# Kernel optimization log

Measured on AMD Instinct MI355X. Metric: run time of the kernel, lower is better.

Reference implementation:

```python
import jax, jax.numpy as jnp
import numpy as np

N, C, T, V, D = 64, 64, 256, 25, 64
BN_EPS = 1e-5


def _make_shift(v, ch, sign):
    idx = np.empty(v * ch, dtype=np.int64)
    for i in range(v):
        for j in range(ch):
            idx[i * ch + j] = (i * ch + j + sign * j * ch) % (ch * v)
    return jnp.asarray(idx, dtype=jnp.int32)


def setup_inputs() -> dict:
    key = jax.random.key(0)
    ks = jax.random.split(key, 8)
    return {
        "x0": jax.random.normal(ks[0], (N, C, T, V), dtype=jnp.float32),
        "fc1_w": jax.random.normal(ks[1], (C // 4, C), dtype=jnp.float32) * (1.0 / np.sqrt(C)),
        "fc1_b": jnp.zeros((C // 4,), dtype=jnp.float32),
        "fc2_w": jax.random.normal(ks[2], (4, C // 4), dtype=jnp.float32) * (1.0 / np.sqrt(C // 4)),
        "fc2_b": jnp.zeros((4,), dtype=jnp.float32),
        "Linear_weight": jax.random.normal(ks[3], (4, C, D), dtype=jnp.float32) * np.sqrt(1.0 / D),
        "Linear_bias": jax.random.normal(ks[4], (4, D), dtype=jnp.float32) * 0.02,
        "Feature_Mask": jax.random.normal(ks[5], (1, V, C), dtype=jnp.float32) * 0.1,
        "bn_gamma": 1.0 + 0.05 * jax.random.normal(ks[6], (V * D,), dtype=jnp.float32),
        "bn_beta": 0.05 * jax.random.normal(ks[7], (V * D,), dtype=jnp.float32),
        "shift_in": _make_shift(V, C, +1),
        "shift_out": _make_shift(V, D, -1),
        "epoch": 100,
    }


def reference(x0, fc1_w, fc1_b, fc2_w, fc2_b, Linear_weight, Linear_bias,
              Feature_Mask, bn_gamma, bn_beta, shift_in, shift_out, epoch):
    n, c, t, v = x0.shape
    d = Linear_weight.shape[-1]

    # DY_SEModule gate: global avg pool -> 1x1 convs -> tempered softmax over 4
    pooled = x0.mean(axis=(2, 3))                       # [n, c]
    h = jax.nn.relu(pooled @ fc1_w.T + fc1_b)           # [n, c//4]
    logits = h @ fc2_w.T + fc2_b                        # [n, 4]
    tao = (-(30.0 - 1.0) / 60.0 * epoch + 30.0) if epoch < 60 else 1.0
    gate = jax.nn.softmax(logits / tao, axis=1)         # [n, 4]

    # per-sample fused weights / bias
    W_fuse = jnp.einsum('kcd,nk->ncd', Linear_weight, gate)   # [n, c, d]
    b_fuse = jnp.einsum('kc,nk->nc', Linear_bias, gate)       # [n, d]

    # shift-in gather over flattened (v*c) channel axis
    x = x0.transpose(0, 2, 3, 1).reshape(n * t, v * c)  # [n*t, v*c]
    x = x[:, shift_in].reshape(n * t, v, c)
    x = x * (jnp.tanh(Feature_Mask) + 1.0)              # learnable feature mask
    x = x.reshape(n, t, v, c)

    # per-sample dynamic linear + bias
    x = jnp.einsum('ntvc,ncd->ntvd', x, W_fuse) + b_fuse[:, None, None, :]

    # shift-out gather
    x = x.reshape(n * t, v * d)[:, shift_out]           # [n*t, v*d]

    # BatchNorm1d (training mode: batch statistics over n*t)
    mean = x.mean(axis=0)
    var = jnp.var(x, axis=0)
    x = (x - mean) * jax.lax.rsqrt(var + BN_EPS) * bn_gamma + bn_beta

    x = x.reshape(n, t, v, d).transpose(0, 3, 1, 2)     # [n, d, t, v]
    return jax.nn.relu(x + x0)                          # identity residual (c == d)
```

## Files before the change

### kernel.cpp

```cpp
#include <hip/hip_runtime.h>
#include <hip/hip_bf16.h>
#include <math.h>

#define NN 64
#define CC 64
#define TT 256
#define VV 25
#define DD 64
#define BN_EPS 1e-5f

typedef short bf16x8 __attribute__((ext_vector_type(8)));
typedef float f32x4 __attribute__((ext_vector_type(4)));

#define WS_POOLED 0
#define WS_GATE   4096
#define WS_BFUSE  4352
#define WS_MASK   8448
#define WS_ABP    10048
#define WS_PART2  13248
#define WS_WTB    218048
#define WS_YB     349120

static __device__ __forceinline__ unsigned short f2bf(float x) {
    __hip_bfloat16 h = __float2bfloat16(x);
    return *(unsigned short*)&h;
}
static __device__ __forceinline__ float bf2f(unsigned short u) {
    return __uint_as_float(((unsigned)u) << 16);
}

__global__ __launch_bounds__(256) void k_mask(const float* __restrict__ fmask, float* ws) {
    const int f = blockIdx.x * 256 + threadIdx.x;
    if (f < VV * CC) ws[WS_MASK + f] = tanhf(fmask[f]) + 1.0f;
}

__global__ __launch_bounds__(256) void k_pool(const float* __restrict__ x0,
                                              float* __restrict__ pooled) {
    __shared__ float red[256];
    const int bid = blockIdx.x;
    const float4* p = (const float4*)(x0 + (size_t)bid * (TT * VV));
    float s = 0.f;
    for (int k = threadIdx.x; k < (TT * VV) / 4; k += 256) {
        float4 v = p[k];
        s += v.x + v.y + v.z + v.w;
    }
    red[threadIdx.x] = s;
    __syncthreads();
    for (int off = 128; off > 0; off >>= 1) {
        if (threadIdx.x < off) red[threadIdx.x] += red[threadIdx.x + off];
        __syncthreads();
    }
    if (threadIdx.x == 0) pooled[bid] = red[0] * (1.f / (TT * VV));
}

__global__ __launch_bounds__(256) void k_gate(const float* __restrict__ fc1_w,
                                              const float* __restrict__ fc1_b,
                                              const float* __restrict__ fc2_w,
                                              const float* __restrict__ fc2_b,
                                              const float* __restrict__ lin_b,
                                              const int* __restrict__ epoch_p,
                                              float* ws) {
    const int tid = threadIdx.x;
    float* pooled = ws + WS_POOLED;
    float* gate   = ws + WS_GATE;
    float* bfuse  = ws + WS_BFUSE;

    if (tid < 64) {
        const int n = tid;
        const float* po = pooled + n * 64;
        float h[16];
        for (int q = 0; q < 16; q++) {
            float z = fc1_b[q];
            for (int j = 0; j < 64; j++) z = fmaf(fc1_w[q * 64 + j], po[j], z);
            h[q] = fmaxf(z, 0.f);
        }
        float lg[4];
        for (int k = 0; k < 4; k++) {
            float z = fc2_b[k];
            for (int q = 0; q < 16; q++) z = fmaf(fc2_w[k * 16 + q], h[q], z);
            lg[k] = z;
        }
        const int ep = epoch_p[0];
        const float tao = (ep < 60) ? (-(29.0f / 60.0f) * (float)ep + 30.0f) : 1.0f;
        float mx = -1e30f;
        for (int k = 0; k < 4; k++) { lg[k] /= tao; mx = fmaxf(mx, lg[k]); }
        float se = 0.f;
        for (int k = 0; k < 4; k++) { lg[k] = expf(lg[k] - mx); se += lg[k]; }
        const float inv = 1.f / se;
        for (int k = 0; k < 4; k++) gate[n * 4 + k] = lg[k] * inv;
    }
    __syncthreads();
    for (int f = tid; f < 4096; f += 256) {
        const int n = f >> 6, d = f & 63;
        float s = 0.f;
        for (int k = 0; k < 4; k++) s = fmaf(lin_b[k * 64 + d], gate[n * 4 + k], s);
        bfuse[f] = s;
    }
}

__global__ __launch_bounds__(256) void k_wfuse(const float* __restrict__ lw, float* ws) {
    __shared__ float tile[64 * 65];
    const float* gate = ws + WS_GATE;
    unsigned short* wtb = (unsigned short*)(ws + WS_WTB);
    const int n = blockIdx.x;
    float g[4];
    for (int k = 0; k < 4; k++) g[k] = gate[n * 4 + k];
    for (int f = threadIdx.x; f < 4096; f += 256) {
        const int c = f >> 6, d = f & 63;
        float v = g[0] * lw[f] + g[1] * lw[4096 + f] + g[2] * lw[8192 + f] + g[3] * lw[12288 + f];
        tile[d * 65 + c] = v;
    }
    __syncthreads();
    for (int f = threadIdx.x; f < 4096; f += 256) {
        const int d = f >> 6, c = f & 63;
        wtb[n * 4096 + f] = f2bf(tile[d * 65 + c]);
    }
}

__global__ __launch_bounds__(256) void k_maing(const float* __restrict__ x0,
                                               const unsigned short* __restrict__ wtb,
                                               const float* __restrict__ ws,
                                               float* __restrict__ wsmut,
                                               float2* __restrict__ scr) {
    __shared__ __align__(16) char pool[35456];
    float* maskL = (float*)pool;
    unsigned short (*Xm)[72] = (unsigned short(*)[72])(pool + 6528);
    const int n = blockIdx.y, tb = blockIdx.x;
    const int tid = threadIdx.x;
    const int wv = tid >> 6, lane = tid & 63;
    const int lrow = lane & 15, lgrp = lane >> 4;
    const int dcol = wv * 16 + lrow;
    unsigned short* outw = (unsigned short*)(pool + 22656) + wv * 1600;

    for (int f = tid; f < 1600; f += 256)
        maskL[(f >> 6) * 65 + (f & 63)] = ws[WS_MASK + f];
    for (int f = tid; f < 864; f += 256) ((unsigned short*)Xm)[7200 + f] = 0;
    const bf16x8 w0 = *(const bf16x8*)(wtb + n * 4096 + dcol * 64 + 8 * lgrp);
    const bf16x8 w1 = *(const bf16x8*)(wtb + n * 4096 + dcol * 64 + 32 + 8 * lgrp);
    const float bfv = ws[WS_BFUSE + n * 64 + dcol];
    __syncthreads();

    float s1r[7][4], s2r[7][4];
#pragma unroll
    for (int m = 0; m < 7; m++)
#pragma unroll
        for (int r = 0; r < 4; r++) { s1r[m][r] = 0.f; s2r[m][r] = 0.f; }

    const size_t nbase = (size_t)n * (CC * TT * VV);
    unsigned short* yg = (unsigned short*)(wsmut + WS_YB) + (size_t)n * 64 * 6400;

    for (int ck = 0; ck < 4; ck++) {
        const int gcol0 = tb * 400 + ck * 100;
        if (ck) __syncthreads();

        for (int l4 = tid; l4 < 1600; l4 += 256) {
            const int j = l4 / 25, q = l4 - j * 25;
            const float4 xv = *(const float4*)(x0 + nbase + j * 6400 + gcol0 + q * 4);
            int jm = j; if (jm >= 50) jm -= 50; else if (jm >= 25) jm -= 25;
            const float xe[4] = {xv.x, xv.y, xv.z, xv.w};
#pragma unroll
            for (int e = 0; e < 4; e++) {
                const int r = q * 4 + e;
                const int trel = (r >= 75) ? 3 : (r >= 50) ? 2 : (r >= 25) ? 1 : 0;
                const int p = r - trel * 25;
                int i = p - jm; if (i < 0) i += 25;
                Xm[trel * 25 + i][j] = f2bf(xe[e] * maskL[i * 65 + j]);
            }
        }
        __syncthreads();

#pragma unroll
        for (int m = 0; m < 7; m++) {
            const bf16x8 a0 = *(const bf16x8*)&Xm[m * 16 + lrow][8 * lgrp];
            const bf16x8 a1 = *(const bf16x8*)&Xm[m * 16 + lrow][32 + 8 * lgrp];
            f32x4 a = {bfv, bfv, bfv, bfv};
            a = __builtin_amdgcn_mfma_f32_16x16x32_bf16(a0, w0, a, 0, 0, 0);
            a = __builtin_amdgcn_mfma_f32_16x16x32_bf16(a1, w1, a, 0, 0, 0);
#pragma unroll
            for (int r = 0; r < 4; r++) {
                const int row = m * 16 + 4 * lgrp + r;
                if (row < 100) {
                    const unsigned short us = f2bf(a[r]);
                    const float yf = bf2f(us);
                    s1r[m][r] += yf;
                    s2r[m][r] = fmaf(yf, yf, s2r[m][r]);
                    outw[lrow * 100 + row] = us;
                }
            }
        }
#pragma unroll
        for (int it = 0; it < 7; it++) {
            const int l = lane + it * 64;
            if (l < 400) {
                const int dloc = l / 25, q = l - dloc * 25;
                const uint2 u = *(const uint2*)(outw + dloc * 100 + 4 * q);
                *(uint2*)(yg + (size_t)(wv * 16 + dloc) * 6400 + gcol0 + 4 * q) = u;
            }
        }
    }

    __syncthreads();
    float* s1l = (float*)pool;
    float* s2l = s1l + 1650;
    for (int f = tid; f < 3300; f += 256) s1l[f] = 0.f;
    __syncthreads();
#pragma unroll
    for (int m = 0; m < 7; m++) {
#pragma unroll
        for (int r = 0; r < 4; r++) {
            const int row = m * 16 + 4 * lgrp + r;
            if (row < 100) {
                int vv = row;
                if (vv >= 75) vv -= 75; else if (vv >= 50) vv -= 50; else if (vv >= 25) vv -= 25;
                __hip_atomic_fetch_add(&s1l[vv * 66 + dcol], s1r[m][r],
                                       __ATOMIC_RELAXED, __HIP_MEMORY_SCOPE_WORKGROUP);
                __hip_atomic_fetch_add(&s2l[vv * 66 + dcol], s2r[m][r],
                                       __ATOMIC_RELAXED, __HIP_MEMORY_SCOPE_WORKGROUP);
            }
        }
    }
    __syncthreads();
    float2* part = scr + (size_t)(n * 16 + tb) * 1600;
    for (int f = tid; f < 1600; f += 256) {
        float2 p;
        p.x = s1l[(f >> 6) * 66 + (f & 63)];
        p.y = s2l[(f >> 6) * 66 + (f & 63)];
        part[f] = p;
    }
}

__global__ __launch_bounds__(256) void k_fred(const float2* __restrict__ scr, float* ws) {
    const int f = blockIdx.x * 256 + threadIdx.x;
    if (f >= VV * DD) return;
    const int slice = blockIdx.y;
    const float2* part = scr + (size_t)slice * 32 * 1600;
    float a0 = 0.f, a1 = 0.f, a2 = 0.f, a3 = 0.f;
    float c0 = 0.f, c1 = 0.f, c2 = 0.f, c3 = 0.f;
#pragma unroll 4
    for (int b = 0; b < 32; b += 4) {
        const float2 p0 = part[(size_t)(b + 0) * 1600 + f];
        const float2 p1 = part[(size_t)(b + 1) * 1600 + f];
        const float2 p2 = part[(size_t)(b + 2) * 1600 + f];
        const float2 p3 = part[(size_t)(b + 3) * 1600 + f];
        a0 += p0.x; c0 += p0.y;
        a1 += p1.x; c1 += p1.y;
        a2 += p2.x; c2 += p2.y;
        a3 += p3.x; c3 += p3.y;
    }
    float2 o;
    o.x = (a0 + a1) + (a2 + a3);
    o.y = (c0 + c1) + (c2 + c3);
    ((float2*)(ws + WS_PART2))[(size_t)slice * 1600 + f] = o;
}

__global__ __launch_bounds__(256) void k_finalize(const float* __restrict__ gamma,
                                                  const float* __restrict__ beta,
                                                  float* ws) {
    const int f = blockIdx.x * 256 + threadIdx.x;
    if (f >= VV * DD) return;
    const int v = f >> 6, d = f & 63;
    const int vi = (v - d + 175) % 25;
    const int fin = vi * 64 + d;

    const float2* part2 = (const float2*)(ws + WS_PART2);
    float a0 = 0.f, a1 = 0.f, a2 = 0.f, a3 = 0.f;
    float c0 = 0.f, c1 = 0.f, c2 = 0.f, c3 = 0.f;
#pragma unroll 4
    for (int b = 0; b < 32; b += 4) {
        const float2 p0 = part2[(size_t)(b + 0) * 1600 + fin];
        const float2 p1 = part2[(size_t)(b + 1) * 1600 + fin];
        const float2 p2 = part2[(size_t)(b + 2) * 1600 + fin];
        const float2 p3 = part2[(size_t)(b + 3) * 1600 + fin];
        a0 += p0.x; c0 += p0.y;
        a1 += p1.x; c1 += p1.y;
        a2 += p2.x; c2 += p2.y;
        a3 += p3.x; c3 += p3.y;
    }
    const float s1 = (a0 + a1) + (a2 + a3);
    const float s2 = (c0 + c1) + (c2 + c3);

    const float mean = s1 * (1.f / (NN * TT));
    float var = s2 * (1.f / (NN * TT)) - mean * mean;
    var = fmaxf(var, 0.f);
    const float rs = rsqrtf(var + BN_EPS);
    const float a = gamma[f] * rs;
    const float b = beta[f] - mean * a;
    ((unsigned*)ws)[WS_ABP + f] = (unsigned)f2bf(a) | (((unsigned)f2bf(b)) << 16);
}

__global__ __launch_bounds__(256) void k_bn(const float* __restrict__ x0,
                                            const float* __restrict__ ws,
                                            float* __restrict__ out) {
    __shared__ __align__(16) unsigned short ybL[6400];
    __shared__ float aL[25], bL[25];
    const int d = blockIdx.x, n = blockIdx.y;
    const int tid = threadIdx.x;
    const size_t pbase = (size_t)(n * 64 + d) * 6400;
    const unsigned short* yb = (const unsigned short*)(ws + WS_YB);

    for (int l = tid; l < 800; l += 256)
        *(uint4*)&ybL[l * 8] = *(const uint4*)(yb + pbase + l * 8);
    if (tid < 25) {
        const unsigned u = ((const unsigned*)ws)[WS_ABP + tid * 64 + d];
        aL[tid] = __uint_as_float(u << 16);
        bL[tid] = __uint_as_float(u & 0xffff0000u);
    }
    __syncthreads();

    const int sh = d % 25;
    for (int l4 = tid; l4 < 1600; l4 += 256) {
        const int e0 = 4 * l4;
        const float4 xv = *(const float4*)(x0 + pbase + e0);
        int t = e0 / 25;
        int vo = e0 - 25 * t;
        float o[4];
        const float xe[4] = {xv.x, xv.y, xv.z, xv.w};
#pragma unroll
        for (int k = 0; k < 4; k++) {
            int vs = vo - sh; if (vs < 0) vs += 25;
            const float y = bf2f(ybL[t * 25 + vs]);
            o[k] = fmaxf(fmaf(aL[vo], y, bL[vo]) + xe[k], 0.f);
            vo++; if (vo >= 25) { vo = 0; t++; }
        }
        float4 ov = {o[0], o[1], o[2], o[3]};
        *(float4*)(out + pbase + e0) = ov;
    }
}

extern "C" void kernel_launch(void* const* d_in, const int* in_sizes, int n_in,
                              void* d_out, int out_size, void* d_ws, size_t ws_size,
                              hipStream_t stream) {
    const float* x0    = (const float*)d_in[0];
    const float* fc1_w = (const float*)d_in[1];
    const float* fc1_b = (const float*)d_in[2];
    const float* fc2_w = (const float*)d_in[3];
    const float* fc2_b = (const float*)d_in[4];
    const float* lw    = (const float*)d_in[5];
    const float* lb    = (const float*)d_in[6];
    const float* fmask = (const float*)d_in[7];
    const float* gamma = (const float*)d_in[8];
    const float* beta  = (const float*)d_in[9];
    const int* epoch   = (const int*)d_in[12];
    float* ws  = (float*)d_ws;
    float* out = (float*)d_out;
    float2* scr = (float2*)d_out;
    const unsigned short* wtb = (const unsigned short*)(ws + WS_WTB);

    k_mask<<<7, 256, 0, stream>>>(fmask, ws);
    k_pool<<<NN * CC, 256, 0, stream>>>(x0, ws + WS_POOLED);
    k_gate<<<1, 256, 0, stream>>>(fc1_w, fc1_b, fc2_w, fc2_b, lb, epoch, ws);
    k_wfuse<<<NN, 256, 0, stream>>>(lw, ws);
    k_maing<<<dim3(16, 64), 256, 0, stream>>>(x0, wtb, ws, ws, scr);
    k_fred<<<dim3(7, 32), 256, 0, stream>>>(scr, ws);
    k_finalize<<<7, 256, 0, stream>>>(gamma, beta, ws);
    k_bn<<<dim3(64, 64), 256, 0, stream>>>(x0, ws, out);
}
```

Before: 208.8 us.

## Batch global loads, fuse mask kernel into gate, use fast bf16 rounding

Folds the tanh feature-mask computation into the single-block gate kernel, which removes one kernel launch. The pooling and main kernels now issue all float4 loads into a register array before consuming them, to raise memory-level parallelism. The library float-to-bf16 conversion is replaced with a plain add-and-shift round, which is cheaper but does not handle NaN, and ties round away from zero instead of to even. The batched loads add register pressure.

Result: faster. 203.5 us (-2.5%).

```diff
diff --git a/kernel.cpp b/kernel.cpp
--- a/kernel.cpp
+++ b/kernel.cpp
@@ -25,13 +25,11 @@
     __hip_bfloat16 h = __float2bfloat16(x);
     return *(unsigned short*)&h;
 }
+static __device__ __forceinline__ unsigned short f2bf_fast(float x) {
+    return (unsigned short)((__float_as_uint(x) + 0x8000u) >> 16);
+}
 static __device__ __forceinline__ float bf2f(unsigned short u) {
     return __uint_as_float(((unsigned)u) << 16);
-}
-
-__global__ __launch_bounds__(256) void k_mask(const float* __restrict__ fmask, float* ws) {
-    const int f = blockIdx.x * 256 + threadIdx.x;
-    if (f < VV * CC) ws[WS_MASK + f] = tanhf(fmask[f]) + 1.0f;
 }
 
 __global__ __launch_bounds__(256) void k_pool(const float* __restrict__ x0,
@@ -39,10 +37,17 @@
     __shared__ float red[256];
     const int bid = blockIdx.x;
     const float4* p = (const float4*)(x0 + (size_t)bid * (TT * VV));
+    float4 xv[7];
+#pragma unroll
+    for (int it = 0; it < 7; it++) {
+        const int k = threadIdx.x + it * 256;
+        if (k < 1600) xv[it] = p[k];
+    }
     float s = 0.f;
-    for (int k = threadIdx.x; k < (TT * VV) / 4; k += 256) {
-        float4 v = p[k];
-        s += v.x + v.y + v.z + v.w;
+#pragma unroll
+    for (int it = 0; it < 7; it++) {
+        const int k = threadIdx.x + it * 256;
+        if (k < 1600) s += xv[it].x + xv[it].y + xv[it].z + xv[it].w;
     }
     red[threadIdx.x] = s;
     __syncthreads();
@@ -58,12 +63,15 @@
                                               const float* __restrict__ fc2_w,
                                               const float* __restrict__ fc2_b,
                                               const float* __restrict__ lin_b,
+                                              const float* __restrict__ fmask,
                                               const int* __restrict__ epoch_p,
                                               float* ws) {
     const int tid = threadIdx.x;
     float* pooled = ws + WS_POOLED;
     float* gate   = ws + WS_GATE;
     float* bfuse  = ws + WS_BFUSE;
+
+    for (int f = tid; f < VV * CC; f += 256) ws[WS_MASK + f] = tanhf(fmask[f]) + 1.0f;
 
     if (tid < 64) {
         const int n = tid;
@@ -153,18 +161,30 @@
         const int gcol0 = tb * 400 + ck * 100;
         if (ck) __syncthreads();
 
-        for (int l4 = tid; l4 < 1600; l4 += 256) {
-            const int j = l4 / 25, q = l4 - j * 25;
-            const float4 xv = *(const float4*)(x0 + nbase + j * 6400 + gcol0 + q * 4);
-            int jm = j; if (jm >= 50) jm -= 50; else if (jm >= 25) jm -= 25;
-            const float xe[4] = {xv.x, xv.y, xv.z, xv.w};
-#pragma unroll
-            for (int e = 0; e < 4; e++) {
-                const int r = q * 4 + e;
-                const int trel = (r >= 75) ? 3 : (r >= 50) ? 2 : (r >= 25) ? 1 : 0;
-                const int p = r - trel * 25;
-                int i = p - jm; if (i < 0) i += 25;
-                Xm[trel * 25 + i][j] = f2bf(xe[e] * maskL[i * 65 + j]);
+        float4 xv[7];
+#pragma unroll
+        for (int it = 0; it < 7; it++) {
+            const int l4 = tid + it * 256;
+            if (l4 < 1600) {
+                const int j = l4 / 25, q = l4 - j * 25;
+                xv[it] = *(const float4*)(x0 + nbase + j * 6400 + gcol0 + q * 4);
+            }
+        }
+#pragma unroll
+        for (int it = 0; it < 7; it++) {
+            const int l4 = tid + it * 256;
+            if (l4 < 1600) {
+                const int j = l4 / 25, q = l4 - j * 25;
+                int jm = j; if (jm >= 50) jm -= 50; else if (jm >= 25) jm -= 25;
+                const float xe[4] = {xv[it].x, xv[it].y, xv[it].z, xv[it].w};
+#pragma unroll
+                for (int e = 0; e < 4; e++) {
+                    const int r = q * 4 + e;
+                    const int trel = (r >= 75) ? 3 : (r >= 50) ? 2 : (r >= 25) ? 1 : 0;
+                    const int p = r - trel * 25;
+                    int i = p - jm; if (i < 0) i += 25;
+                    Xm[trel * 25 + i][j] = f2bf_fast(xe[e] * maskL[i * 65 + j]);
+                }
             }
         }
         __syncthreads();
@@ -180,7 +200,7 @@
             for (int r = 0; r < 4; r++) {
                 const int row = m * 16 + 4 * lgrp + r;
                 if (row < 100) {
-                    const unsigned short us = f2bf(a[r]);
+                    const unsigned short us = f2bf_fast(a[r]);
                     const float yf = bf2f(us);
                     s1r[m][r] += yf;
                     s2r[m][r] = fmaf(yf, yf, s2r[m][r]);
@@ -346,9 +366,8 @@
     float2* scr = (float2*)d_out;
     const unsigned short* wtb = (const unsigned short*)(ws + WS_WTB);
 
-    k_mask<<<7, 256, 0, stream>>>(fmask, ws);
     k_pool<<<NN * CC, 256, 0, stream>>>(x0, ws + WS_POOLED);
-    k_gate<<<1, 256, 0, stream>>>(fc1_w, fc1_b, fc2_w, fc2_b, lb, epoch, ws);
+    k_gate<<<1, 256, 0, stream>>>(fc1_w, fc1_b, fc2_w, fc2_b, lb, fmask, epoch, ws);
     k_wfuse<<<NN, 256, 0, stream>>>(lw, ws);
     k_maing<<<dim3(16, 64), 256, 0, stream>>>(x0, wtb, ws, ws, scr);
     k_fred<<<dim3(7, 32), 256, 0, stream>>>(scr, ws);
```
